# Kernel tuning notes

Measured on AMD Instinct MI355X. Metric: run time of the kernel, lower is better.

The kernel has to match this reference:

```python
import jax, jax.numpy as jnp
import numpy as np

B, C, L = 32, 64, 2048
SA_KQ = 50

def setup_inputs() -> dict:
    key = jax.random.key(0)
    ks = jax.random.split(key, 7)
    return {
        "x": jax.random.normal(ks[0], (B, C, L), dtype=jnp.float32),
        "Wk": jax.random.normal(ks[1], (C, SA_KQ), dtype=jnp.float32) * 0.1,
        "bk": jax.random.normal(ks[2], (SA_KQ,), dtype=jnp.float32) * 0.1,
        "Wq": jax.random.normal(ks[3], (C, SA_KQ), dtype=jnp.float32) * 0.1,
        "bq": jax.random.normal(ks[4], (SA_KQ,), dtype=jnp.float32) * 0.1,
        "Wv": jax.random.normal(ks[5], (C, C), dtype=jnp.float32) * 0.1,
        "bv": jax.random.normal(ks[6], (C,), dtype=jnp.float32) * 0.1,
        "sample_len": 128,
    }

def reference(x, Wk, bk, Wq, bq, Wv, bv, sample_len):
    # x: [B, C, L] -> permute(0,2,1) -> [B, L, C]
    xt = jnp.transpose(x, (0, 2, 1))
    # Dropout is identity in eval mode.
    k = jax.nn.elu(xt @ Wk + bk)          # [B, L, 50]
    q = jax.nn.elu(xt @ Wq + bq)          # [B, L, 50]
    v = jnp.tanh(xt @ Wv + bv)            # [B, L, 64]
    scale = 1.0 / jnp.sqrt(jnp.float32(sample_len))
    w = jnp.einsum('bld,bmd->blm', k, q) * scale   # [B, L, L]
    w = jax.nn.softmax(w, axis=1)         # softmax over dim=1 (non-standard)
    y = jnp.einsum('blm,bmc->blc', w, v)  # [B, L, 64]
    return y
```

## Files before the change

### kernel.cpp

```cpp
#include <hip/hip_runtime.h>
#include <math.h>

#define B_  32
#define L_  2048
#define D_  64
#define LOG2E 1.44269504088896340736f

typedef unsigned short u16;
typedef unsigned int u32;
typedef float f32x4 __attribute__((ext_vector_type(4)));
typedef short s16x8 __attribute__((ext_vector_type(8)));
typedef __fp16 h16x2 __attribute__((ext_vector_type(2)));
typedef _Float16 f16x8 __attribute__((ext_vector_type(8)));

__device__ inline int swz(int row, int blk) { return blk ^ (row & 7); }

__device__ inline float scalar_as_float(const int* p) {
    int v = *p;
    return (v > 0 && v < (1 << 23)) ? (float)v : __int_as_float(v);
}
__device__ inline float fexp2(float x) {
#if __has_builtin(__builtin_amdgcn_exp2f)
    return __builtin_amdgcn_exp2f(x);
#else
    return exp2f(x);
#endif
}
__device__ inline float frcp(float x) {
#if __has_builtin(__builtin_amdgcn_rcpf)
    return __builtin_amdgcn_rcpf(x);
#else
    return 1.0f / x;
#endif
}
__device__ inline float fast_elu(float a) {
    return a > 0.f ? a : fexp2(a * LOG2E) - 1.0f;
}
__device__ inline float fast_tanh(float a) {
    a = fminf(fmaxf(a, -20.f), 20.f);
    const float t = fexp2(a * (2.0f * LOG2E));
    return (t - 1.0f) * frcp(t + 1.0f);
}
__device__ inline u32 cvt_pk_f16(float a, float b) {
    union { h16x2 h; u32 u; } cv;
    cv.h = __builtin_amdgcn_cvt_pkrtz(a, b);
    return cv.u;
}
__device__ inline u32 cvt_pk_bf16(float a, float b) {
    u32 r;
    asm("v_cvt_pk_bf16_f32 %0, %1, %2" : "=v"(r) : "v"(a), "v"(b));
    return r;
}
__device__ inline f32x4 mfma_bf(s16x8 a, s16x8 b, f32x4 c) {
    return __builtin_amdgcn_mfma_f32_16x16x32_bf16(a, b, c, 0, 0, 0);
}
__device__ inline f32x4 mfma_h(f16x8 a, f16x8 b, f32x4 c) {
    return __builtin_amdgcn_mfma_f32_16x16x32_f16(a, b, c, 0, 0, 0);
}

__global__ __launch_bounds__(256)
void kqv_kernel(const float* __restrict__ x,
                const float* __restrict__ Wk, const float* __restrict__ bk,
                const float* __restrict__ Wq, const float* __restrict__ bq,
                const float* __restrict__ Wv, const float* __restrict__ bv,
                const int* __restrict__ slen,
                u16* __restrict__ Kf, u16* __restrict__ Qf,
                u16* __restrict__ Vt)
{
    __shared__ __align__(16) float xs[64 * 65];
    __shared__ __align__(16) u16 ah[64 * 64];
    __shared__ __align__(16) u16 wh[64 * 64];
    __shared__ float bsh[192];

    const int t = threadIdx.x;
    const int b = blockIdx.y;
    const int l0 = blockIdx.x * 64;
    const int wave = t >> 6;
    const int lane = t & 63;
    const int l15 = lane & 15;
    const int quad = lane >> 4;

    #pragma unroll
    for (int it = 0; it < 4; ++it) {
        const int c = (t >> 4) + it * 16;
        const int l4 = (t & 15) * 4;
        const float4 v = *(const float4*)&x[((size_t)b * 64 + c) * L_ + l0 + l4];
        xs[(l4 + 0) * 65 + c] = v.x;
        xs[(l4 + 1) * 65 + c] = v.y;
        xs[(l4 + 2) * 65 + c] = v.z;
        xs[(l4 + 3) * 65 + c] = v.w;
    }
    if (t < 64)       bsh[t] = (t < 50) ? bk[t] : 0.f;
    else if (t < 128) bsh[t] = (t - 64 < 50) ? bq[t - 64] : 0.f;
    else if (t < 192) bsh[t] = bv[t - 128];
    __syncthreads();

    {
        const int l = t >> 2, sg = t & 3;
        const float* xr = &xs[l * 65 + sg * 16];
        union { u32 w[4]; uint4 v; } H0, H1;
        #pragma unroll
        for (int p = 0; p < 4; ++p) {
            H0.w[p] = cvt_pk_f16(xr[2 * p],     xr[2 * p + 1]);
            H1.w[p] = cvt_pk_f16(xr[8 + 2 * p], xr[9 + 2 * p]);
        }
        *(uint4*)(ah + l * 64 + (swz(l, 2 * sg) << 3))     = H0.v;
        *(uint4*)(ah + l * 64 + (swz(l, 2 * sg + 1) << 3)) = H1.v;
    }
    __syncthreads();

    const int arow = wave * 16 + l15;
    const f16x8 a0 = *(const f16x8*)(ah + arow * 64 + (swz(arow, quad) << 3));
    const f16x8 a1 = *(const f16x8*)(ah + arow * 64 + (swz(arow, quad | 4) << 3));

    const float sc2 = rsqrtf(scalar_as_float(slen)) * LOG2E;

    for (int ph = 0; ph < 3; ++ph) {
        __syncthreads();
        {
            const int ch = t & 63, c0 = wave * 16;
            const float* W = (ph == 0) ? Wk : (ph == 1) ? Wq : Wv;
            const int wd = (ph == 2) ? 64 : 50;
            #pragma unroll
            for (int j = 0; j < 16; j += 2) {
                const int c = c0 + j;
                const float w0 = (ch < wd) ? W[c * wd + ch] : 0.f;
                const float w1 = (ch < wd) ? W[(c + 1) * wd + ch] : 0.f;
                const int idx = ch * 64 + (swz(ch, c >> 3) << 3) + (c & 7);
                *(u32*)(wh + idx) = cvt_pk_f16(w0, w1);
            }
        }
        __syncthreads();

        #pragma unroll
        for (int ct = 0; ct < 4; ++ct) {
            const int brow = ct * 16 + l15;
            const f16x8 b0 = *(const f16x8*)(wh + brow * 64 + (swz(brow, quad) << 3));
            const f16x8 b1 = *(const f16x8*)(wh + brow * 64 + (swz(brow, quad | 4) << 3));
            const float bb = bsh[ph * 64 + brow];
            f32x4 c = {bb, bb, bb, bb};
            c = mfma_h(a0, b0, c);
            c = mfma_h(a1, b1, c);

            const size_t off0 = ((size_t)b * L_ + l0 + wave * 16 + quad * 4) * D_ + brow;
            if (ph == 0) {
                const u32 k01 = cvt_pk_f16(fast_elu(c[0]), fast_elu(c[1]));
                const u32 k23 = cvt_pk_f16(fast_elu(c[2]), fast_elu(c[3]));
                Kf[off0]          = (u16)k01;
                Kf[off0 + D_]     = (u16)(k01 >> 16);
                Kf[off0 + 2 * D_] = (u16)k23;
                Kf[off0 + 3 * D_] = (u16)(k23 >> 16);
            } else if (ph == 1) {
                const u32 q01 = cvt_pk_f16(fast_elu(c[0]) * sc2, fast_elu(c[1]) * sc2);
                const u32 q23 = cvt_pk_f16(fast_elu(c[2]) * sc2, fast_elu(c[3]) * sc2);
                Qf[off0]          = (u16)q01;
                Qf[off0 + D_]     = (u16)(q01 >> 16);
                Qf[off0 + 2 * D_] = (u16)q23;
                Qf[off0 + 3 * D_] = (u16)(q23 >> 16);
            } else {
                uint2 pv;
                pv.x = cvt_pk_bf16(fast_tanh(c[0]), fast_tanh(c[1]));
                pv.y = cvt_pk_bf16(fast_tanh(c[2]), fast_tanh(c[3]));
                const size_t off = ((size_t)b * 64 + brow) * L_ + l0 + wave * 16 + quad * 4;
                *(uint2*)(Vt + off) = pv;
            }
        }
    }
}

__global__ __launch_bounds__(256, 4)
void zsum_kernel(const u16* __restrict__ Kf, const u16* __restrict__ Qf,
                 u16* __restrict__ Vt)
{
    __shared__ __align__(16) u16 kh_s[64 * 64];
    __shared__ float zs[64];

    const int t = threadIdx.x;
    const int b = blockIdx.y;
    const int m0 = blockIdx.x * 64;
    const int wave = t >> 6;
    const int lane = t & 63;
    const int l15 = lane & 15;
    const int quad = lane >> 4;
    const int r = t >> 2, sg = t & 3;

    const size_t qrow = ((size_t)b * L_ + m0 + wave * 16 + l15) * D_;
    const f16x8 q0 = *(const f16x8*)(Qf + qrow + quad * 8);
    const f16x8 q1 = *(const f16x8*)(Qf + qrow + 32 + quad * 8);

    float zacc[4] = {0.f, 0.f, 0.f, 0.f};

    uint4 rk0, rk1;
    {
        const size_t kb = ((size_t)b * L_ + r) * D_ + sg * 16;
        rk0 = *(const uint4*)(Kf + kb); rk1 = *(const uint4*)(Kf + kb + 8);
    }
    const int lo0 = r * 64 + (swz(r, 2 * sg) << 3);
    const int lo1 = r * 64 + (swz(r, 2 * sg + 1) << 3);

    for (int ch = 0; ch < 32; ++ch) {
        __syncthreads();
        *(uint4*)(kh_s + lo0) = rk0;  *(uint4*)(kh_s + lo1) = rk1;
        __syncthreads();
        if (ch < 31) {
            const size_t kb = ((size_t)b * L_ + (ch + 1) * 64 + r) * D_ + sg * 16;
            rk0 = *(const uint4*)(Kf + kb); rk1 = *(const uint4*)(Kf + kb + 8);
        }
        #pragma unroll
        for (int lt = 0; lt < 4; ++lt) {
            const int row = lt * 16 + l15;
            const f16x8 b0 = *(const f16x8*)(kh_s + row * 64 + (swz(row, quad) << 3));
            const f16x8 b1 = *(const f16x8*)(kh_s + row * 64 + (swz(row, quad | 4) << 3));
            f32x4 s = {0.f, 0.f, 0.f, 0.f};
            s = mfma_h(q0, b0, s);
            s = mfma_h(q1, b1, s);
            #pragma unroll
            for (int i = 0; i < 4; ++i)
                zacc[i] += fexp2(fminf(s[i], 80.f));
        }
    }

    #pragma unroll
    for (int off = 1; off < 16; off <<= 1)
        #pragma unroll
        for (int i = 0; i < 4; ++i)
            zacc[i] += __shfl_xor(zacc[i], off, 64);

    if (l15 == 0) {
        #pragma unroll
        for (int i = 0; i < 4; ++i)
            zs[wave * 16 + quad * 4 + i] = frcp(fmaxf(zacc[i], 1e-30f));
    }
    __syncthreads();

    {
        const size_t vb = ((size_t)b * 64 + r) * L_ + m0 + sg * 16;
        union { u16 s[16]; u32 w[8]; uint4 v[2]; } V;
        V.v[0] = *(const uint4*)(Vt + vb);
        V.v[1] = *(const uint4*)(Vt + vb + 8);
        #pragma unroll
        for (int p = 0; p < 8; ++p) {
            const float f0 = __uint_as_float((u32)V.s[2 * p]     << 16) * zs[sg * 16 + 2 * p];
            const float f1 = __uint_as_float((u32)V.s[2 * p + 1] << 16) * zs[sg * 16 + 2 * p + 1];
            V.w[p] = cvt_pk_bf16(f0, f1);
        }
        *(uint4*)(Vt + vb)     = V.v[0];
        *(uint4*)(Vt + vb + 8) = V.v[1];
    }
}

__global__ __launch_bounds__(256, 4)
void out_kernel(const u16* __restrict__ Kf, const u16* __restrict__ Qf,
                const u16* __restrict__ Vt, float* __restrict__ out)
{
    __shared__ __align__(16) u16 qh_s[64 * 64];
    __shared__ __align__(16) u16 vn_s[64 * 64];
    __shared__ __align__(16) u16 ph_s[4][16 * 64];

    const int t = threadIdx.x;
    const int b = blockIdx.y;
    const int l0 = blockIdx.x * 64;
    const int wave = t >> 6;
    const int lane = t & 63;
    const int l15 = lane & 15;
    const int quad = lane >> 4;
    const int r = t >> 2, sg = t & 3;
    u16* const ph = ph_s[wave];

    const size_t krow = ((size_t)b * L_ + l0 + wave * 16 + l15) * D_;
    const f16x8 k0 = *(const f16x8*)(Kf + krow + quad * 8);
    const f16x8 k1 = *(const f16x8*)(Kf + krow + 32 + quad * 8);

    f32x4 acc[4];
    #pragma unroll
    for (int ct = 0; ct < 4; ++ct) acc[ct] = (f32x4){0.f, 0.f, 0.f, 0.f};

    uint4 rq0, rq1, rv0, rv1;
    {
        const size_t qb = ((size_t)b * L_ + r) * D_ + sg * 16;
        const size_t vb = ((size_t)b * 64 + r) * L_ + sg * 16;
        rq0 = *(const uint4*)(Qf + qb);  rq1 = *(const uint4*)(Qf + qb + 8);
        rv0 = *(const uint4*)(Vt + vb);  rv1 = *(const uint4*)(Vt + vb + 8);
    }
    const int lo0 = r * 64 + (swz(r, 2 * sg) << 3);
    const int lo1 = r * 64 + (swz(r, 2 * sg + 1) << 3);

    for (int ch = 0; ch < 32; ++ch) {
        __syncthreads();
        *(uint4*)(qh_s + lo0) = rq0; *(uint4*)(qh_s + lo1) = rq1;
        *(uint4*)(vn_s + lo0) = rv0; *(uint4*)(vn_s + lo1) = rv1;
        __syncthreads();
        if (ch < 31) {
            const size_t qb = ((size_t)b * L_ + (ch + 1) * 64 + r) * D_ + sg * 16;
            const size_t vb = ((size_t)b * 64 + r) * L_ + (ch + 1) * 64 + sg * 16;
            rq0 = *(const uint4*)(Qf + qb);  rq1 = *(const uint4*)(Qf + qb + 8);
            rv0 = *(const uint4*)(Vt + vb);  rv1 = *(const uint4*)(Vt + vb + 8);
        }

        #pragma unroll
        for (int mt = 0; mt < 4; ++mt) {
            const int row = mt * 16 + l15;
            const f16x8 a0 = *(const f16x8*)(qh_s + row * 64 + (swz(row, quad) << 3));
            const f16x8 a1 = *(const f16x8*)(qh_s + row * 64 + (swz(row, quad | 4) << 3));
            f32x4 s = {0.f, 0.f, 0.f, 0.f};
            s = mfma_h(a0, k0, s);
            s = mfma_h(a1, k1, s);
            uint2 p2;
            p2.x = cvt_pk_bf16(fexp2(fminf(s[0], 80.f)), fexp2(fminf(s[1], 80.f)));
            p2.y = cvt_pk_bf16(fexp2(fminf(s[2], 80.f)), fexp2(fminf(s[3], 80.f)));
            const int pw = l15 * 64 + (swz(l15, 2 * mt + (quad >> 1)) << 3) + (quad & 1) * 4;
            *(uint2*)(ph + pw) = p2;
        }

        #pragma unroll
        for (int ks = 0; ks < 2; ++ks) {
            const s16x8 pa = *(const s16x8*)(ph + l15 * 64 + (swz(l15, 4 * ks + quad) << 3));
            #pragma unroll
            for (int ct = 0; ct < 4; ++ct) {
                const int vrow = ct * 16 + l15;
                const s16x8 bvh = *(const s16x8*)(vn_s + vrow * 64 + (swz(vrow, 4 * ks + quad) << 3));
                acc[ct] = mfma_bf(pa, bvh, acc[ct]);
            }
        }
    }

    const int row = l0 + wave * 16 + quad * 4;
    #pragma unroll
    for (int ct = 0; ct < 4; ++ct)
        #pragma unroll
        for (int i = 0; i < 4; ++i)
            out[((size_t)b * L_ + row + i) * 64 + ct * 16 + l15] = acc[ct][i];
}

extern "C" void kernel_launch(void* const* d_in, const int* in_sizes, int n_in,
                              void* d_out, int out_size, void* d_ws, size_t ws_size,
                              hipStream_t stream)
{
    const float* x  = (const float*)d_in[0];
    const float* Wk = (const float*)d_in[1];
    const float* bk = (const float*)d_in[2];
    const float* Wq = (const float*)d_in[3];
    const float* bq = (const float*)d_in[4];
    const float* Wv = (const float*)d_in[5];
    const float* bv = (const float*)d_in[6];
    const int* slen = (const int*)d_in[7];
    float* out = (float*)d_out;

    const size_t n = (size_t)B_ * L_ * D_;
    u16* Kf = (u16*)d_ws;
    u16* Qf = Kf + n;
    u16* Vt = Qf + n;

    kqv_kernel<<<dim3(L_ / 64, B_), 256, 0, stream>>>(x, Wk, bk, Wq, bq, Wv, bv,
                                                      slen, Kf, Qf, Vt);
    zsum_kernel<<<dim3(L_ / 64, B_), 256, 0, stream>>>(Kf, Qf, Vt);
    out_kernel<<<dim3(L_ / 64, B_), 256, 0, stream>>>(Kf, Qf, Vt, out);
}
```

Before: 180.2 us.

## Read Q and V tiles directly from global memory instead of LDS staging

Removes the shared-memory staging buffers for Q and V, along with the register prefetch of the next chunk and one block-wide barrier. Each wave now loads its MFMA operands straight from global memory, relying on the caches to serve the repeated reads. The aim is to cut LDS writes, barrier cost and LDS footprint, which may allow more resident blocks. The cost is that all four waves fetch the same Q/V data from global memory, and with no prefetch the load latency sits directly in the compute loop. A sched_barrier is also added between the two MFMA phases.

New measurement: 350.8 us. 94.6% more time.

```diff
diff --git a/kernel.cpp b/kernel.cpp
--- a/kernel.cpp
+++ b/kernel.cpp
@@ -253,8 +253,6 @@
 void out_kernel(const u16* __restrict__ Kf, const u16* __restrict__ Qf,
                 const u16* __restrict__ Vt, float* __restrict__ out)
 {
-    __shared__ __align__(16) u16 qh_s[64 * 64];
-    __shared__ __align__(16) u16 vn_s[64 * 64];
     __shared__ __align__(16) u16 ph_s[4][16 * 64];
 
     const int t = threadIdx.x;
@@ -264,7 +262,6 @@
     const int lane = t & 63;
     const int l15 = lane & 15;
     const int quad = lane >> 4;
-    const int r = t >> 2, sg = t & 3;
     u16* const ph = ph_s[wave];
 
     const size_t krow = ((size_t)b * L_ + l0 + wave * 16 + l15) * D_;
@@ -275,33 +272,17 @@
     #pragma unroll
     for (int ct = 0; ct < 4; ++ct) acc[ct] = (f32x4){0.f, 0.f, 0.f, 0.f};
 
-    uint4 rq0, rq1, rv0, rv1;
-    {
-        const size_t qb = ((size_t)b * L_ + r) * D_ + sg * 16;
-        const size_t vb = ((size_t)b * 64 + r) * L_ + sg * 16;
-        rq0 = *(const uint4*)(Qf + qb);  rq1 = *(const uint4*)(Qf + qb + 8);
-        rv0 = *(const uint4*)(Vt + vb);  rv1 = *(const uint4*)(Vt + vb + 8);
-    }
-    const int lo0 = r * 64 + (swz(r, 2 * sg) << 3);
-    const int lo1 = r * 64 + (swz(r, 2 * sg + 1) << 3);
+    const u16* qbase = Qf + (size_t)b * L_ * D_;
+    const u16* vbase = Vt + (size_t)b * 64 * L_;
 
     for (int ch = 0; ch < 32; ++ch) {
         __syncthreads();
-        *(uint4*)(qh_s + lo0) = rq0; *(uint4*)(qh_s + lo1) = rq1;
-        *(uint4*)(vn_s + lo0) = rv0; *(uint4*)(vn_s + lo1) = rv1;
-        __syncthreads();
-        if (ch < 31) {
-            const size_t qb = ((size_t)b * L_ + (ch + 1) * 64 + r) * D_ + sg * 16;
-            const size_t vb = ((size_t)b * 64 + r) * L_ + (ch + 1) * 64 + sg * 16;
-            rq0 = *(const uint4*)(Qf + qb);  rq1 = *(const uint4*)(Qf + qb + 8);
-            rv0 = *(const uint4*)(Vt + vb);  rv1 = *(const uint4*)(Vt + vb + 8);
-        }
 
         #pragma unroll
         for (int mt = 0; mt < 4; ++mt) {
-            const int row = mt * 16 + l15;
-            const f16x8 a0 = *(const f16x8*)(qh_s + row * 64 + (swz(row, quad) << 3));
-            const f16x8 a1 = *(const f16x8*)(qh_s + row * 64 + (swz(row, quad | 4) << 3));
+            const u16* qr = qbase + (size_t)(ch * 64 + mt * 16 + l15) * D_;
+            const f16x8 a0 = *(const f16x8*)(qr + quad * 8);
+            const f16x8 a1 = *(const f16x8*)(qr + 32 + quad * 8);
             f32x4 s = {0.f, 0.f, 0.f, 0.f};
             s = mfma_h(a0, k0, s);
             s = mfma_h(a1, k1, s);
@@ -312,13 +293,17 @@
             *(uint2*)(ph + pw) = p2;
         }
 
+        __builtin_amdgcn_sched_barrier(0);
+
         #pragma unroll
         for (int ks = 0; ks < 2; ++ks) {
-            const s16x8 pa = *(const s16x8*)(ph + l15 * 64 + (swz(l15, 4 * ks + quad) << 3));
+            union { uint4 u; s16x8 s; } pa_u;
+            pa_u.u = *(const uint4*)(ph + l15 * 64 + (swz(l15, 4 * ks + quad) << 3));
+            const s16x8 pa = pa_u.s;
             #pragma unroll
             for (int ct = 0; ct < 4; ++ct) {
-                const int vrow = ct * 16 + l15;
-                const s16x8 bvh = *(const s16x8*)(vn_s + vrow * 64 + (swz(vrow, 4 * ks + quad) << 3));
+                const u16* vr = vbase + (size_t)(ct * 16 + l15) * L_ + ch * 64;
+                const s16x8 bvh = *(const s16x8*)(vr + ks * 32 + quad * 8);
                 acc[ct] = mfma_bf(pa, bvh, acc[ct]);
             }
         }
```
